# Kernel tuning notes

Hardware: AMD Instinct MI355X
Metric: run time of the kernel (lower is better)

Reference implementation:

```python
import jax, jax.numpy as jnp
import numpy as np


def setup_inputs() -> dict:
    key = jax.random.key(0)
    B = 64          # number of utterances (segments)
    N = 16384       # total frames = sum(segment_num)
    D = 1024        # embedding_size
    A = 2048        # attention_dim
    H = 8           # attention_head_num
    k1, k2, k3, k4 = jax.random.split(key, 4)
    # ragged segment lengths, all >= 1, summing exactly to N
    rng = np.random.default_rng(0)
    lens = rng.integers(64, 512, size=B).astype(np.float64)
    lens = np.maximum(1, (lens * N / lens.sum()).astype(np.int64))
    lens[-1] += N - lens.sum()
    assert lens.sum() == N and (lens > 0).all()
    segment_num = jnp.asarray(lens, dtype=jnp.int32)
    x = jax.random.normal(k1, (N, D), jnp.float32)
    # torch Linear weights, stored pre-transposed as [in, out]
    w1 = jax.random.normal(k2, (D, A), jnp.float32) / np.sqrt(D)
    w2 = jax.random.normal(k3, (A, H), jnp.float32) / np.sqrt(A)
    # post_fc: Linear(D*H -> D, bias=False), stored as [D*H, D]
    w_post = jax.random.normal(k4, (D * H, D), jnp.float32) / np.sqrt(D * H)
    return {"x": x, "segment_num": segment_num, "w1": w1, "w2": w2, "w_post": w_post}


def reference(x, segment_num, w1, w2, w_post):
    N, D = x.shape
    B = segment_num.shape[0]
    H = w2.shape[1]
    # segment id for every frame (ragged -> flat segment ids)
    seg_ids = jnp.repeat(jnp.arange(B), segment_num, total_repeat_length=N)  # [N]

    # MultiAtt.w1: Linear -> ReLU -> Linear, per frame
    h = jnp.maximum(x @ w1, 0.0) @ w2  # [N, H]

    # per-segment softmax over the time axis (dim 0 within each segment)
    m = jax.ops.segment_max(h, seg_ids, num_segments=B)          # [B, H]
    p = jnp.exp(h - m[seg_ids])                                  # [N, H]
    s = jax.ops.segment_sum(p, seg_ids, num_segments=B)          # [B, H]
    attn = p / s[seg_ids]                                        # [N, H]

    # per-segment x^T @ attn -> [B, D, H] (matches torch.mm(x.T, attn))
    out_bdh = jax.ops.segment_sum(x[:, :, None] * attn[:, None, :], seg_ids, num_segments=B)
    # flatten row-major over (D, H) like out.view(-1), then post_fc (no bias)
    out = out_bdh.reshape(B, D * H) @ w_post                     # [B, D]

    # attn_i = attn^T @ attn per segment -> [B, H, H]
    attn_gram = jax.ops.segment_sum(attn[:, :, None] * attn[:, None, :], seg_ids, num_segments=B)

    # segment_type == 'average': per-segment mean of frames -> [B, D]
    out_segment = jax.ops.segment_sum(x, seg_ids, num_segments=B) / segment_num[:, None].astype(x.dtype)

    return out, out_segment, attn_gram
```

## Files before the change

kernel.cpp:

```cpp
#include <hip/hip_runtime.h>
#include <hip/hip_bf16.h>

#define NB 64
#define NN 16384
#define ND 1024
#define NA 2048
#define NH 8
#define NSLOT 16
#define KSPL 64
#define NPL 16

typedef __attribute__((ext_vector_type(4))) float f32x4;
typedef __attribute__((ext_vector_type(8))) short short8;
typedef __attribute__((ext_vector_type(8))) unsigned short ushort8;

__device__ __forceinline__ unsigned short f2bf(float f) {
    unsigned int u = __float_as_uint(f);
    u = (u + 0x7fff + ((u >> 16) & 1)) >> 16;
    return (unsigned short)u;
}

__device__ __forceinline__ float bf2f(unsigned short s) {
    return __uint_as_float((unsigned int)s << 16);
}

__device__ __forceinline__ void load_lds16(const void* g, void* l) {
    __builtin_amdgcn_global_load_lds((const __attribute__((address_space(1))) void*)g,
                                     (__attribute__((address_space(3))) void*)l, 16, 0, 0);
}

__global__ __launch_bounds__(256) void k_pre(const float* __restrict__ x,
                                             const float* __restrict__ w1,
                                             const int* __restrict__ segnum,
                                             unsigned short* __restrict__ xb,
                                             unsigned short* __restrict__ w1t,
                                             int* __restrict__ segoff) {
    __shared__ unsigned short t[32][33];
    const int bx = blockIdx.x;
    if (bx < 8192) {
        size_t i = ((size_t)bx * 256 + threadIdx.x) * 8;
        float4 a = *(const float4*)(x + i);
        float4 b = *(const float4*)(x + i + 4);
        ushort8 o;
        o[0] = f2bf(a.x); o[1] = f2bf(a.y); o[2] = f2bf(a.z); o[3] = f2bf(a.w);
        o[4] = f2bf(b.x); o[5] = f2bf(b.y); o[6] = f2bf(b.z); o[7] = f2bf(b.w);
        *(ushort8*)(xb + i) = o;
    } else if (bx < 10240) {
        const int idx = bx - 8192;
        const int a0 = (idx & 63) * 32, d0 = (idx >> 6) * 32;
        const int tx = threadIdx.x & 31, ty4 = (threadIdx.x >> 5) * 4;
#pragma unroll
        for (int i = 0; i < 4; i++)
            t[tx][ty4 + i] = f2bf(w1[(size_t)(d0 + ty4 + i) * NA + a0 + tx]);
        __syncthreads();
#pragma unroll
        for (int i = 0; i < 4; i++)
            w1t[(size_t)(a0 + ty4 + i) * ND + d0 + tx] = t[ty4 + i][tx];
    } else {
        if (threadIdx.x == 0) {
            int a = 0;
            segoff[0] = 0;
            for (int b = 0; b < NB; b++) { a += segnum[b]; segoff[b + 1] = a; }
        }
    }
}

__global__ __launch_bounds__(256) void k_c1h(const unsigned short* __restrict__ xb,
                                             const unsigned short* __restrict__ w1t,
                                             const float* __restrict__ w2,
                                             float* __restrict__ h_part) {
    __shared__ unsigned short SM[21760];
    unsigned short* As  = SM;
    unsigned short* Bs  = SM + 8192;
    unsigned short* c1s = SM;
    unsigned short* w2hi = SM + 17408;
    unsigned short* w2lo = SM + 19584;

    const int tid = threadIdx.x;
    const int wave = tid >> 6, lane = tid & 63;
    const int wm = wave & 1, wn = wave >> 1;
    const int m0 = blockIdx.x * 128, n0 = blockIdx.y * 128;
    const int quad = lane >> 4, lc = lane & 15;

    for (int i = tid; i < 2176; i += 256) { w2hi[i] = 0; w2lo[i] = 0; }
    for (int i = tid; i < 1024; i += 256) {
        int k = i >> 3, q = i & 7;
        float w = w2[(size_t)(n0 + k) * NH + q];
        unsigned short hi = f2bf(w);
        w2hi[q * 136 + k] = hi;
        w2lo[q * 136 + k] = f2bf(w - bf2f(hi));
    }

    f32x4 acc[4][4];
#pragma unroll
    for (int i = 0; i < 4; i++)
#pragma unroll
        for (int j = 0; j < 4; j++) acc[i][j] = (f32x4){0.f, 0.f, 0.f, 0.f};

    const int srow = lane >> 3;
    const int sg = lane & 7;

    for (int k0 = 0; k0 < ND; k0 += 64) {
        __syncthreads();
#pragma unroll
        for (int i = 0; i < 4; i++) {
            int r = wave * 32 + i * 8 + srow;
            int gc = (sg ^ (r & 7)) * 8;
            load_lds16(xb + (size_t)(m0 + r) * ND + k0 + gc, As + r * 64 + sg * 8);
            load_lds16(w1t + (size_t)(n0 + r) * ND + k0 + gc, Bs + r * 64 + sg * 8);
        }
        __syncthreads();
#pragma unroll
        for (int ksub = 0; ksub < 2; ksub++) {
            short8 af[4], bf[4];
            const int lg = ksub * 4 + quad;
#pragma unroll
            for (int t = 0; t < 4; t++) {
                int m = wm * 64 + t * 16 + lc;
                af[t] = *(const short8*)&As[m * 64 + (lg ^ (m & 7)) * 8];
                int n = wn * 64 + t * 16 + lc;
                bf[t] = *(const short8*)&Bs[n * 64 + (lg ^ (n & 7)) * 8];
            }
#pragma unroll
            for (int mi = 0; mi < 4; mi++)
#pragma unroll
                for (int ni = 0; ni < 4; ni++)
                    acc[mi][ni] = __builtin_amdgcn_mfma_f32_16x16x32_bf16(
                        af[mi], bf[ni], acc[mi][ni], 0, 0, 0);
        }
    }

    __syncthreads();
#pragma unroll
    for (int mi = 0; mi < 4; mi++)
#pragma unroll
        for (int ni = 0; ni < 4; ni++) {
            const int col = wn * 64 + ni * 16 + lc;
#pragma unroll
            for (int r = 0; r < 4; r++) {
                const int row = wm * 64 + mi * 16 + quad * 4 + r;
                c1s[row * 136 + col] = f2bf(fmaxf(acc[mi][ni][r], 0.f));
            }
        }
    __syncthreads();

    f32x4 hacc[2];
    hacc[0] = (f32x4){0.f, 0.f, 0.f, 0.f};
    hacc[1] = (f32x4){0.f, 0.f, 0.f, 0.f};
#pragma unroll
    for (int ks = 0; ks < 4; ks++) {
        short8 bh = *(const short8*)&w2hi[lc * 136 + ks * 32 + quad * 8];
        short8 bl = *(const short8*)&w2lo[lc * 136 + ks * 32 + quad * 8];
#pragma unroll
        for (int mt = 0; mt < 2; mt++) {
            short8 af = *(const short8*)&c1s[(wave * 32 + mt * 16 + lc) * 136 + ks * 32 + quad * 8];
            hacc[mt] = __builtin_amdgcn_mfma_f32_16x16x32_bf16(af, bh, hacc[mt], 0, 0, 0);
            hacc[mt] = __builtin_amdgcn_mfma_f32_16x16x32_bf16(af, bl, hacc[mt], 0, 0, 0);
        }
    }

    if (lc < NH) {
        float* hp = h_part + (size_t)blockIdx.y * (NN * NH);
#pragma unroll
        for (int mt = 0; mt < 2; mt++)
#pragma unroll
            for (int r = 0; r < 4; r++)
                hp[(size_t)(m0 + wave * 32 + mt * 16 + quad * 4 + r) * NH + lc] = hacc[mt][r];
    }
}

__global__ __launch_bounds__(256) void k_attn(const float* __restrict__ h_part,
                                              float* __restrict__ attn,
                                              const int* __restrict__ segoff,
                                              float* __restrict__ gram) {
    const int b = blockIdx.x;
    const int s0 = segoff[b], s1 = segoff[b + 1];
    const int len = s1 - s0;
    const int tid = threadIdx.x;
    const int wv = tid >> 6;
    __shared__ float hl[1024 * NH];
    __shared__ float red[4][NH];
    __shared__ float mb[NH];
    __shared__ float sinv[NH];
    __shared__ float gred[4][64];

    float mx[NH];
#pragma unroll
    for (int q = 0; q < NH; q++) mx[q] = -1e30f;

    const bool cached = (len <= 1024);

    for (int n = s0 + tid; n < s1; n += 256) {
        float v[NH];
#pragma unroll
        for (int q = 0; q < NH; q++) v[q] = 0.f;
#pragma unroll
        for (int p = 0; p < NPL; p++) {
            const float4* hp = (const float4*)(h_part + (size_t)p * (NN * NH) + (size_t)n * NH);
            float4 u0 = hp[0], u1 = hp[1];
            v[0] += u0.x; v[1] += u0.y; v[2] += u0.z; v[3] += u0.w;
            v[4] += u1.x; v[5] += u1.y; v[6] += u1.z; v[7] += u1.w;
        }
        if (cached) {
#pragma unroll
            for (int q = 0; q < NH; q++) hl[(n - s0) * NH + q] = v[q];
        }
#pragma unroll
        for (int q = 0; q < NH; q++) mx[q] = fmaxf(mx[q], v[q]);
    }
#pragma unroll
    for (int q = 0; q < NH; q++)
        for (int o = 1; o < 64; o <<= 1) mx[q] = fmaxf(mx[q], __shfl_xor(mx[q], o));
    if ((tid & 63) == 0)
        for (int q = 0; q < NH; q++) red[wv][q] = mx[q];
    __syncthreads();
    if (tid < NH)
        mb[tid] = fmaxf(fmaxf(red[0][tid], red[1][tid]), fmaxf(red[2][tid], red[3][tid]));
    __syncthreads();

    float sm[NH];
#pragma unroll
    for (int q = 0; q < NH; q++) sm[q] = 0.f;
    for (int n = s0 + tid; n < s1; n += 256) {
        float v[NH];
        if (cached) {
#pragma unroll
            for (int q = 0; q < NH; q++) v[q] = hl[(n - s0) * NH + q];
        } else {
#pragma unroll
            for (int q = 0; q < NH; q++) v[q] = 0.f;
#pragma unroll
            for (int p = 0; p < NPL; p++) {
                const float4* hp = (const float4*)(h_part + (size_t)p * (NN * NH) + (size_t)n * NH);
                float4 u0 = hp[0], u1 = hp[1];
                v[0] += u0.x; v[1] += u0.y; v[2] += u0.z; v[3] += u0.w;
                v[4] += u1.x; v[5] += u1.y; v[6] += u1.z; v[7] += u1.w;
            }
        }
#pragma unroll
        for (int q = 0; q < NH; q++) sm[q] += expf(v[q] - mb[q]);
    }
#pragma unroll
    for (int q = 0; q < NH; q++)
        for (int o = 1; o < 64; o <<= 1) sm[q] += __shfl_xor(sm[q], o);
    if ((tid & 63) == 0)
        for (int q = 0; q < NH; q++) red[wv][q] = sm[q];
    __syncthreads();
    if (tid < NH)
        sinv[tid] = 1.0f / (red[0][tid] + red[1][tid] + red[2][tid] + red[3][tid]);
    __syncthreads();

    float g[NH][NH];
#pragma unroll
    for (int i = 0; i < NH; i++)
#pragma unroll
        for (int j = 0; j < NH; j++) g[i][j] = 0.f;

    for (int n = s0 + tid; n < s1; n += 256) {
        float v[NH];
        if (cached) {
#pragma unroll
            for (int q = 0; q < NH; q++) v[q] = hl[(n - s0) * NH + q];
        } else {
#pragma unroll
            for (int q = 0; q < NH; q++) v[q] = 0.f;
#pragma unroll
            for (int p = 0; p < NPL; p++) {
                const float4* hp = (const float4*)(h_part + (size_t)p * (NN * NH) + (size_t)n * NH);
                float4 u0 = hp[0], u1 = hp[1];
                v[0] += u0.x; v[1] += u0.y; v[2] += u0.z; v[3] += u0.w;
                v[4] += u1.x; v[5] += u1.y; v[6] += u1.z; v[7] += u1.w;
            }
        }
        float a[NH];
        float* ar = &attn[(size_t)n * NH];
#pragma unroll
        for (int q = 0; q < NH; q++) { a[q] = expf(v[q] - mb[q]) * sinv[q]; ar[q] = a[q]; }
#pragma unroll
        for (int i = 0; i < NH; i++)
#pragma unroll
            for (int j = 0; j < NH; j++) g[i][j] += a[i] * a[j];
    }
#pragma unroll
    for (int i = 0; i < NH; i++)
#pragma unroll
        for (int j = 0; j < NH; j++)
            for (int o = 1; o < 64; o <<= 1) g[i][j] += __shfl_xor(g[i][j], o);

    if ((tid & 63) == 0) {
#pragma unroll
        for (int i = 0; i < NH; i++)
#pragma unroll
            for (int j = 0; j < NH; j++) gred[wv][i * NH + j] = g[i][j];
    }
    __syncthreads();
    if (tid < 64)
        gram[(size_t)b * 64 + tid] = gred[0][tid] + gred[1][tid] + gred[2][tid] + gred[3][tid];
}

__global__ __launch_bounds__(128) void k_bdh(const unsigned short* __restrict__ xb,
                                             const float* __restrict__ attn,
                                             const int* __restrict__ segoff,
                                             float* __restrict__ bdh_part,
                                             float* __restrict__ xsum_part) {
    const int slot = blockIdx.x;
    const int b = blockIdx.y;
    const int s0 = segoff[b], s1 = segoff[b + 1];
    const int dl = threadIdx.x;

    float acc[8][NH];
    float xs[8];
#pragma unroll
    for (int dd = 0; dd < 8; dd++) {
        xs[dd] = 0.f;
#pragma unroll
        for (int q = 0; q < NH; q++) acc[dd][q] = 0.f;
    }

    for (int n = s0 + slot; n < s1; n += NSLOT) {
        ushort8 xv = *(const ushort8*)(xb + (size_t)n * ND + dl * 8);
        const float4* ap = (const float4*)&attn[(size_t)n * NH];
        float4 a0 = ap[0], a1 = ap[1];
        float aq[NH] = {a0.x, a0.y, a0.z, a0.w, a1.x, a1.y, a1.z, a1.w};
#pragma unroll
        for (int dd = 0; dd < 8; dd++) {
            float xf = bf2f(xv[dd]);
            xs[dd] += xf;
#pragma unroll
            for (int q = 0; q < NH; q++) acc[dd][q] += xf * aq[q];
        }
    }

    float* bp = bdh_part + ((size_t)slot * NB + b) * (ND * NH) + (size_t)dl * 64;
#pragma unroll
    for (int dd = 0; dd < 8; dd++) {
        *(float4*)(bp + dd * 8)     = make_float4(acc[dd][0], acc[dd][1], acc[dd][2], acc[dd][3]);
        *(float4*)(bp + dd * 8 + 4) = make_float4(acc[dd][4], acc[dd][5], acc[dd][6], acc[dd][7]);
    }
    float* xp = xsum_part + ((size_t)slot * NB + b) * ND + (size_t)dl * 8;
    *(float4*)(xp)     = make_float4(xs[0], xs[1], xs[2], xs[3]);
    *(float4*)(xp + 4) = make_float4(xs[4], xs[5], xs[6], xs[7]);
}

__global__ __launch_bounds__(256) void k_bdh_red(const float* __restrict__ bdh_part,
                                                 const float* __restrict__ xsum_part,
                                                 const int* __restrict__ segoff,
                                                 float* __restrict__ bdh,
                                                 float* __restrict__ out_segment) {
    const int gid = blockIdx.x * 256 + threadIdx.x;
    const int b = gid >> 10, d = gid & 1023;
    float4 sa = make_float4(0.f, 0.f, 0.f, 0.f);
    float4 sb = make_float4(0.f, 0.f, 0.f, 0.f);
    float xsum = 0.f;
#pragma unroll
    for (int s = 0; s < NSLOT; s++) {
        const float* p = bdh_part + ((size_t)s * NB + b) * (ND * NH) + (size_t)d * NH;
        float4 u = ((const float4*)p)[0], v = ((const float4*)p)[1];
        sa.x += u.x; sa.y += u.y; sa.z += u.z; sa.w += u.w;
        sb.x += v.x; sb.y += v.y; sb.z += v.z; sb.w += v.w;
        xsum += xsum_part[((size_t)s * NB + b) * ND + d];
    }
    float* bp = bdh + (size_t)b * (ND * NH) + (size_t)d * NH;
    ((float4*)bp)[0] = sa;
    ((float4*)bp)[1] = sb;
    const int len = segoff[b + 1] - segoff[b];
    out_segment[(size_t)b * ND + d] = xsum / (float)len;
}

__global__ __launch_bounds__(256) void k_post(const float* __restrict__ bdh,
                                              const float* __restrict__ wp,
                                              float* __restrict__ out_part) {
    __shared__ float as[32][68];
    __shared__ float bs[32][128];
    const int tid = threadIdx.x;
    const int n0 = blockIdx.x * 128;
    const int k0 = blockIdx.y * (8192 / KSPL);
    const int tr = tid >> 4, tc = tid & 15;

    float acc[4][8];
#pragma unroll
    for (int i = 0; i < 4; i++)
#pragma unroll
        for (int j = 0; j < 8; j++) acc[i][j] = 0.f;

    for (int kc = 0; kc < 8192 / KSPL; kc += 32) {
        __syncthreads();
        {
            int r = tid >> 2;
            int c = (tid & 3) * 8;
            const float4* gp = (const float4*)(bdh + (size_t)r * (ND * NH) + k0 + kc + c);
            float4 v0 = gp[0], v1 = gp[1];
            as[c + 0][r] = v0.x; as[c + 1][r] = v0.y; as[c + 2][r] = v0.z; as[c + 3][r] = v0.w;
            as[c + 4][r] = v1.x; as[c + 5][r] = v1.y; as[c + 6][r] = v1.z; as[c + 7][r] = v1.w;
        }
        {
            int r = tid >> 3;
            int c = (tid & 7) * 16;
            const float4* gp = (const float4*)(wp + (size_t)(k0 + kc + r) * ND + n0 + c);
            float4* sp = (float4*)&bs[r][c];
            sp[0] = gp[0]; sp[1] = gp[1]; sp[2] = gp[2]; sp[3] = gp[3];
        }
        __syncthreads();
#pragma unroll
        for (int k = 0; k < 32; k++) {
            float4 a  = *(const float4*)&as[k][tr * 4];
            float4 b0 = *(const float4*)&bs[k][tc * 8];
            float4 b1 = *(const float4*)&bs[k][tc * 8 + 4];
            float av[4] = {a.x, a.y, a.z, a.w};
            float bv[8] = {b0.x, b0.y, b0.z, b0.w, b1.x, b1.y, b1.z, b1.w};
#pragma unroll
            for (int i = 0; i < 4; i++)
#pragma unroll
                for (int j = 0; j < 8; j++) acc[i][j] += av[i] * bv[j];
        }
    }

    float* op = out_part + (size_t)blockIdx.y * (NB * ND);
#pragma unroll
    for (int i = 0; i < 4; i++)
#pragma unroll
        for (int j = 0; j < 8; j++)
            op[(size_t)(tr * 4 + i) * ND + n0 + tc * 8 + j] = acc[i][j];
}

__global__ __launch_bounds__(256) void k_post_red(const float* __restrict__ out_part,
                                                  float* __restrict__ out) {
    const int i = (blockIdx.x * 256 + threadIdx.x) * 4;
    float4 s = *(const float4*)(out_part + i);
#pragma unroll
    for (int p = 1; p < KSPL; p++) {
        float4 v = *(const float4*)(out_part + (size_t)p * (NB * ND) + i);
        s.x += v.x; s.y += v.y; s.z += v.z; s.w += v.w;
    }
    *(float4*)(out + i) = s;
}

extern "C" void kernel_launch(void* const* d_in, const int* in_sizes, int n_in,
                              void* d_out, int out_size, void* d_ws, size_t ws_size,
                              hipStream_t stream) {
    (void)in_sizes; (void)n_in; (void)out_size; (void)ws_size;
    const float* x      = (const float*)d_in[0];
    const int*   segnum = (const int*)d_in[1];
    const float* w1     = (const float*)d_in[2];
    const float* w2     = (const float*)d_in[3];
    const float* wpost  = (const float*)d_in[4];

    float* out         = (float*)d_out;
    float* out_segment = out + NB * ND;
    float* gram        = out + 2 * NB * ND;

    char* ws = (char*)d_ws;
    const size_t MB = 1024 * 1024;
    int*   segoff   = (int*)ws;
    float* attn     = (float*)(ws + 1 * MB);
    float* bdh      = (float*)(ws + 2 * MB);
    float* h_part   = (float*)(ws + 4 * MB);
    unsigned short* xb  = (unsigned short*)(ws + 12 * MB);
    unsigned short* w1t = (unsigned short*)(ws + 44 * MB);
    float* bdh_part  = (float*)(ws + 48 * MB);
    float* xsum_part = (float*)(ws + 80 * MB);
    float* out_part  = (float*)(ws + 84 * MB);

    k_pre<<<10241, 256, 0, stream>>>(x, w1, segnum, xb, w1t, segoff);
    k_c1h<<<dim3(NN / 128, NA / 128), 256, 0, stream>>>(xb, w1t, w2, h_part);
    k_attn<<<NB, 256, 0, stream>>>(h_part, attn, segoff, gram);
    k_bdh<<<dim3(NSLOT, NB), 128, 0, stream>>>(xb, attn, segoff, bdh_part, xsum_part);
    k_bdh_red<<<256, 256, 0, stream>>>(bdh_part, xsum_part, segoff, bdh, out_segment);
    k_post<<<dim3(ND / 128, KSPL), 256, 0, stream>>>(bdh, wpost, out_part);
    k_post_red<<<(NB * ND) / (256 * 4), 256, 0, stream>>>(out_part, out);
}
```

Baseline: 283.2 us.

## Rework first-layer GEMM into 256x256 tiles with software-pipelined LDS staging

After: 262.3 us. 1.08x faster.

```diff
diff --git a/kernel.cpp b/kernel.cpp
--- a/kernel.cpp
+++ b/kernel.cpp
@@ -8,7 +8,8 @@
 #define NH 8
 #define NSLOT 16
 #define KSPL 64
-#define NPL 16
+#define NPL 8
+#define NT 16
 
 typedef __attribute__((ext_vector_type(4))) float f32x4;
 typedef __attribute__((ext_vector_type(8))) short short8;
@@ -65,98 +66,176 @@
     }
 }
 
-__global__ __launch_bounds__(256) void k_c1h(const unsigned short* __restrict__ xb,
-                                             const unsigned short* __restrict__ w1t,
-                                             const float* __restrict__ w2,
-                                             float* __restrict__ h_part) {
-    __shared__ unsigned short SM[21760];
-    unsigned short* As  = SM;
-    unsigned short* Bs  = SM + 8192;
-    unsigned short* c1s = SM;
-    unsigned short* w2hi = SM + 17408;
-    unsigned short* w2lo = SM + 19584;
+__global__ __launch_bounds__(512, 2) void k_c1h(const unsigned short* __restrict__ xb,
+                                                const unsigned short* __restrict__ w1t,
+                                                const float* __restrict__ w2,
+                                                float* __restrict__ h_part) {
+    __shared__ unsigned short SM[73984];
+    unsigned short* As   = SM;
+    unsigned short* Bs   = SM + 32768;
+    unsigned short* w2hi = SM + 65536;
+    unsigned short* w2lo = SM + 69760;
 
     const int tid = threadIdx.x;
-    const int wave = tid >> 6, lane = tid & 63;
-    const int wm = wave & 1, wn = wave >> 1;
-    const int m0 = blockIdx.x * 128, n0 = blockIdx.y * 128;
+    const int wv = tid >> 6, lane = tid & 63;
+    const int wm = wv >> 2, wn = wv & 3;
     const int quad = lane >> 4, lc = lane & 15;
-
-    for (int i = tid; i < 2176; i += 256) { w2hi[i] = 0; w2lo[i] = 0; }
-    for (int i = tid; i < 1024; i += 256) {
+    const int l7 = lc & 7;
+    const int m0 = blockIdx.x * 256, n0 = blockIdx.y * 256;
+
+    for (int i = tid; i < 4224; i += 512) { w2hi[i] = 0; w2lo[i] = 0; }
+    for (int i = tid; i < 2048; i += 512) {
         int k = i >> 3, q = i & 7;
         float w = w2[(size_t)(n0 + k) * NH + q];
         unsigned short hi = f2bf(w);
-        w2hi[q * 136 + k] = hi;
-        w2lo[q * 136 + k] = f2bf(w - bf2f(hi));
-    }
-
-    f32x4 acc[4][4];
-#pragma unroll
-    for (int i = 0; i < 4; i++)
+        w2hi[q * 264 + k] = hi;
+        w2lo[q * 264 + k] = f2bf(w - bf2f(hi));
+    }
+
+    const int rr = wv * 8 + (lane >> 3);
+    const size_t goff0 = (size_t)rr * ND + (size_t)(((lane & 7) ^ (lane >> 3)) << 3);
+    const size_t goff1 = goff0 + (size_t)64 * ND;
+    const int ls0 = wv * 512, ls1 = (wv + 8) * 512;
+
+    const unsigned short* xA = xb  + (size_t)m0 * ND;
+    const unsigned short* xB = w1t + (size_t)n0 * ND;
+
+#define STAGE(SRC, DST) do { \
+        load_lds16((SRC) + goff0, (DST) + ls0); \
+        load_lds16((SRC) + goff1, (DST) + ls1); } while (0)
+
+    f32x4 acc[8][4];
+#pragma unroll
+    for (int i = 0; i < 8; i++)
 #pragma unroll
         for (int j = 0; j < 4; j++) acc[i][j] = (f32x4){0.f, 0.f, 0.f, 0.f};
 
-    const int srow = lane >> 3;
-    const int sg = lane & 7;
-
-    for (int k0 = 0; k0 < ND; k0 += 64) {
-        __syncthreads();
-#pragma unroll
-        for (int i = 0; i < 4; i++) {
-            int r = wave * 32 + i * 8 + srow;
-            int gc = (sg ^ (r & 7)) * 8;
-            load_lds16(xb + (size_t)(m0 + r) * ND + k0 + gc, As + r * 64 + sg * 8);
-            load_lds16(w1t + (size_t)(n0 + r) * ND + k0 + gc, Bs + r * 64 + sg * 8);
-        }
-        __syncthreads();
-#pragma unroll
-        for (int ksub = 0; ksub < 2; ksub++) {
-            short8 af[4], bf[4];
-            const int lg = ksub * 4 + quad;
-#pragma unroll
-            for (int t = 0; t < 4; t++) {
-                int m = wm * 64 + t * 16 + lc;
-                af[t] = *(const short8*)&As[m * 64 + (lg ^ (m & 7)) * 8];
-                int n = wn * 64 + t * 16 + lc;
-                bf[t] = *(const short8*)&Bs[n * 64 + (lg ^ (n & 7)) * 8];
-            }
-#pragma unroll
-            for (int mi = 0; mi < 4; mi++)
-#pragma unroll
-                for (int ni = 0; ni < 4; ni++)
-                    acc[mi][ni] = __builtin_amdgcn_mfma_f32_16x16x32_bf16(
-                        af[mi], bf[ni], acc[mi][ni], 0, 0, 0);
-        }
-    }
-
-    __syncthreads();
-#pragma unroll
-    for (int mi = 0; mi < 4; mi++)
-#pragma unroll
-        for (int ni = 0; ni < 4; ni++) {
-            const int col = wn * 64 + ni * 16 + lc;
-#pragma unroll
-            for (int r = 0; r < 4; r++) {
-                const int row = wm * 64 + mi * 16 + quad * 4 + r;
-                c1s[row * 136 + col] = f2bf(fmaxf(acc[mi][ni][r], 0.f));
-            }
-        }
-    __syncthreads();
-
+    int aoff[4], boff[2];
+#pragma unroll
+    for (int i = 0; i < 4; i++) aoff[i] = (wm * 64 + i * 16 + lc) * 64;
+#pragma unroll
+    for (int i = 0; i < 2; i++) boff[i] = (wn * 32 + i * 16 + lc) * 64;
+
+#define PHASE(D, MU, NU, STAGES, WAIT2)                                          \
+    do {                                                                         \
+        const unsigned short* Ab = As + ((D) * 2 + (MU)) * 8192;                 \
+        const unsigned short* Bb = Bs + ((D) * 2 + (NU)) * 8192;                 \
+        short8 af[4][2], bfr[2][2];                                              \
+        _Pragma("unroll") for (int i = 0; i < 4; i++) {                          \
+            af[i][0] = *(const short8*)&Ab[aoff[i] + ((quad ^ l7) << 3)];        \
+            af[i][1] = *(const short8*)&Ab[aoff[i] + (((4 + quad) ^ l7) << 3)];  \
+        }                                                                        \
+        _Pragma("unroll") for (int i = 0; i < 2; i++) {                          \
+            bfr[i][0] = *(const short8*)&Bb[boff[i] + ((quad ^ l7) << 3)];       \
+            bfr[i][1] = *(const short8*)&Bb[boff[i] + (((4 + quad) ^ l7) << 3)]; \
+        }                                                                        \
+        STAGES;                                                                  \
+        asm volatile("" ::: "memory");                                           \
+        __builtin_amdgcn_s_barrier();                                            \
+        asm volatile("" ::: "memory");                                           \
+        __builtin_amdgcn_s_setprio(1);                                           \
+        _Pragma("unroll") for (int i = 0; i < 4; i++)                            \
+            _Pragma("unroll") for (int j = 0; j < 2; j++) {                      \
+                acc[(MU) * 4 + i][(NU) * 2 + j] =                                \
+                    __builtin_amdgcn_mfma_f32_16x16x32_bf16(                     \
+                        af[i][0], bfr[j][0], acc[(MU) * 4 + i][(NU) * 2 + j],    \
+                        0, 0, 0);                                                \
+                acc[(MU) * 4 + i][(NU) * 2 + j] =                                \
+                    __builtin_amdgcn_mfma_f32_16x16x32_bf16(                     \
+                        af[i][1], bfr[j][1], acc[(MU) * 4 + i][(NU) * 2 + j],    \
+                        0, 0, 0);                                                \
+            }                                                                    \
+        __builtin_amdgcn_s_setprio(0);                                           \
+        WAIT2;                                                                   \
+        asm volatile("" ::: "memory");                                           \
+        __builtin_amdgcn_s_barrier();                                            \
+        asm volatile("" ::: "memory");                                           \
+    } while (0)
+
+    STAGE(xA, As);
+    STAGE(xB, Bs);
+    STAGE(xA + (size_t)128 * ND, As + 8192);
+    STAGE(xB + (size_t)128 * ND, Bs + 8192);
+    STAGE(xA + 64, As + 16384);
+    STAGE(xB + 64, Bs + 16384);
+    asm volatile("s_waitcnt vmcnt(4)" ::: "memory");
+    __builtin_amdgcn_s_barrier();
+    asm volatile("" ::: "memory");
+
+#pragma unroll 2
+    for (int t = 0; t < NT - 2; t++) {
+        const int d = t & 1;
+        const unsigned short* xAn = xA + (t + 1) * 64;
+        const unsigned short* xBn = xB + (t + 1) * 64;
+        const unsigned short* xAnn = xA + (t + 2) * 64;
+        const unsigned short* xBnn = xB + (t + 2) * 64;
+        unsigned short* Ad1 = As + ((d ^ 1) * 2) * 8192;
+        unsigned short* Bd1 = Bs + ((d ^ 1) * 2) * 8192;
+        unsigned short* Ad2 = As + (d * 2) * 8192;
+        unsigned short* Bd2 = Bs + (d * 2) * 8192;
+        PHASE(d, 0, 0,
+              { STAGE(xAn + (size_t)128 * ND, Ad1 + 8192);
+                STAGE(xBn + (size_t)128 * ND, Bd1 + 8192); }, {});
+        PHASE(d, 0, 1, {}, {});
+        PHASE(d, 1, 0, { STAGE(xAnn, Ad2); }, {});
+        PHASE(d, 1, 1, { STAGE(xBnn, Bd2); },
+              { asm volatile("s_waitcnt vmcnt(4)" ::: "memory"); });
+    }
+    {
+        const unsigned short* xAn = xA + (NT - 1) * 64;
+        const unsigned short* xBn = xB + (NT - 1) * 64;
+        PHASE(0, 0, 0,
+              { STAGE(xAn + (size_t)128 * ND, As + 3 * 8192);
+                STAGE(xBn + (size_t)128 * ND, Bs + 3 * 8192); }, {});
+        PHASE(0, 0, 1, {}, {});
+        PHASE(0, 1, 0, {}, {});
+        PHASE(0, 1, 1, {}, { asm volatile("s_waitcnt vmcnt(0)" ::: "memory"); });
+    }
+    PHASE(1, 0, 0, {}, {});
+    PHASE(1, 0, 1, {}, {});
+    PHASE(1, 1, 0, {}, {});
+    PHASE(1, 1, 1, {}, {});
+
+#undef PHASE
+#undef STAGE
+
+    unsigned short* c1s = SM;
     f32x4 hacc[2];
     hacc[0] = (f32x4){0.f, 0.f, 0.f, 0.f};
     hacc[1] = (f32x4){0.f, 0.f, 0.f, 0.f};
-#pragma unroll
-    for (int ks = 0; ks < 4; ks++) {
-        short8 bh = *(const short8*)&w2hi[lc * 136 + ks * 32 + quad * 8];
-        short8 bl = *(const short8*)&w2lo[lc * 136 + ks * 32 + quad * 8];
-#pragma unroll
-        for (int mt = 0; mt < 2; mt++) {
-            short8 af = *(const short8*)&c1s[(wave * 32 + mt * 16 + lc) * 136 + ks * 32 + quad * 8];
-            hacc[mt] = __builtin_amdgcn_mfma_f32_16x16x32_bf16(af, bh, hacc[mt], 0, 0, 0);
-            hacc[mt] = __builtin_amdgcn_mfma_f32_16x16x32_bf16(af, bl, hacc[mt], 0, 0, 0);
-        }
+
+#pragma unroll
+    for (int nu = 0; nu < 2; nu++) {
+#pragma unroll
+        for (int mi = 0; mi < 8; mi++) {
+            const int row = (mi >> 2) * 128 + wm * 64 + (mi & 3) * 16 + quad * 4;
+#pragma unroll
+            for (int nj = 0; nj < 2; nj++) {
+                const int col = wn * 32 + nj * 16 + lc;
+                const int ni = nu * 2 + nj;
+#pragma unroll
+                for (int r = 0; r < 4; r++)
+                    c1s[(row + r) * 136 + col] = f2bf(fmaxf(acc[mi][ni][r], 0.f));
+            }
+        }
+        asm volatile("s_waitcnt lgkmcnt(0)" ::: "memory");
+        __builtin_amdgcn_s_barrier();
+        asm volatile("" ::: "memory");
+#pragma unroll
+        for (int ks = 0; ks < 4; ks++) {
+            short8 bh = *(const short8*)&w2hi[lc * 264 + nu * 128 + ks * 32 + quad * 8];
+            short8 bl = *(const short8*)&w2lo[lc * 264 + nu * 128 + ks * 32 + quad * 8];
+#pragma unroll
+            for (int mt = 0; mt < 2; mt++) {
+                short8 afr = *(const short8*)&c1s[(wv * 32 + mt * 16 + lc) * 136 +
+                                                  ks * 32 + quad * 8];
+                hacc[mt] = __builtin_amdgcn_mfma_f32_16x16x32_bf16(afr, bh, hacc[mt], 0, 0, 0);
+                hacc[mt] = __builtin_amdgcn_mfma_f32_16x16x32_bf16(afr, bl, hacc[mt], 0, 0, 0);
+            }
+        }
+        asm volatile("" ::: "memory");
+        __builtin_amdgcn_s_barrier();
+        asm volatile("" ::: "memory");
     }
 
     if (lc < NH) {
@@ -165,7 +244,7 @@
         for (int mt = 0; mt < 2; mt++)
 #pragma unroll
             for (int r = 0; r < 4; r++)
-                hp[(size_t)(m0 + wave * 32 + mt * 16 + quad * 4 + r) * NH + lc] = hacc[mt][r];
+                hp[(size_t)(m0 + wv * 32 + mt * 16 + quad * 4 + r) * NH + lc] = hacc[mt][r];
     }
 }
 
@@ -462,7 +541,7 @@
     float* out_part  = (float*)(ws + 84 * MB);
 
     k_pre<<<10241, 256, 0, stream>>>(x, w1, segnum, xb, w1t, segoff);
-    k_c1h<<<dim3(NN / 128, NA / 128), 256, 0, stream>>>(xb, w1t, w2, h_part);
+    k_c1h<<<dim3(NN / 256, NA / 256), 512, 0, stream>>>(xb, w1t, w2, h_part);
     k_attn<<<NB, 256, 0, stream>>>(h_part, attn, segoff, gram);
     k_bdh<<<dim3(NSLOT, NB), 128, 0, stream>>>(xb, attn, segoff, bdh_part, xsum_part);
     k_bdh_red<<<256, 256, 0, stream>>>(bdh_part, xsum_part, segoff, bdh, out_segment);
```
